# Kernel optimization log

Measured on AMD Instinct MI355X. Metric: run time of the kernel, lower is better.

## Reference

```python
import jax, jax.numpy as jnp
import numpy as np

C_IN = 256
C_INT = C_IN // 2  # inter_channels


def _conv1x1(x, w, b):
    # x: [B, Cin, H, W], w: [Cout, Cin], b: [Cout]
    return jnp.einsum('bchw,oc->bohw', x, w) + b[None, :, None, None]


def setup_inputs() -> dict:
    key = jax.random.key(0)
    ks = jax.random.split(key, 9)
    B, H, W = 8, 64, 64
    s_in = 1.0 / np.sqrt(C_IN)
    s_int = 1.0 / np.sqrt(C_INT)
    return {
        'x': jax.random.normal(ks[0], (B, C_IN, H, W), dtype=jnp.float32),
        'g_w': jax.random.normal(ks[1], (C_INT, C_IN), dtype=jnp.float32) * s_in,
        'g_b': jax.random.normal(ks[2], (C_INT,), dtype=jnp.float32) * s_in,
        'theta_w': jax.random.normal(ks[3], (C_INT, C_IN), dtype=jnp.float32) * s_in,
        'theta_b': jax.random.normal(ks[4], (C_INT,), dtype=jnp.float32) * s_in,
        'phi_w': jax.random.normal(ks[5], (C_INT, C_IN), dtype=jnp.float32) * s_in,
        'phi_b': jax.random.normal(ks[6], (C_INT,), dtype=jnp.float32) * s_in,
        'W_w': jax.random.normal(ks[7], (C_IN, C_INT), dtype=jnp.float32) * s_int,
        'W_b': jax.random.normal(ks[8], (C_IN,), dtype=jnp.float32) * s_int,
    }


def reference(x, g_w, g_b, theta_w, theta_b, phi_w, phi_b, W_w, W_b):
    B, C, H, W = x.shape
    N = H * W
    g_x = _conv1x1(x, g_w, g_b).reshape(B, C_INT, N)        # [B, Ci, N]
    theta_x = _conv1x1(x, theta_w, theta_b).reshape(B, C_INT, N)
    phi_x = _conv1x1(x, phi_w, phi_b).reshape(B, C_INT, N)
    # f[b, i, j] = theta[:, i] . phi[:, j]  (no scaling, per original)
    f = jnp.einsum('bci,bcj->bij', theta_x, phi_x)          # [B, N, N]
    f_div_C = jax.nn.softmax(f, axis=-1)
    y = jnp.einsum('bij,bcj->bci', f_div_C, g_x)            # [B, Ci, N]
    y = y.reshape(B, C_INT, H, W)
    y = _conv1x1(y, W_w, W_b)                               # [B, C, H, W]
    return x + y
```

## Files before the change

### kernel.cpp

```cpp
#include <hip/hip_runtime.h>

typedef _Float16 f16;
typedef _Float16 f16x4 __attribute__((ext_vector_type(4)));
typedef _Float16 f16x8 __attribute__((ext_vector_type(8)));
typedef float f32x4 __attribute__((ext_vector_type(4)));
typedef float f32x16 __attribute__((ext_vector_type(16)));

#define MFMA16(a, b, c) __builtin_amdgcn_mfma_f32_16x16x32_f16(a, b, c, 0, 0, 0)
#define MFMA32(a, b, c) __builtin_amdgcn_mfma_f32_32x32x16_f16(a, b, c, 0, 0, 0)

__device__ __forceinline__ int swzr(int row) { return ((row & 7) << 4) ^ ((row & 8) << 2); }

__global__ __launch_bounds__(256) void wcvt_k(
    const float* __restrict__ tw, const float* __restrict__ pw,
    const float* __restrict__ gw, const float* __restrict__ ww,
    f16* __restrict__ Wall, f16* __restrict__ Wepi) {
  int i = blockIdx.x * 256 + threadIdx.x;
  if (i < 384 * 256) {
    int c = i >> 8, cp = i & 255;
    float v = (c < 128) ? tw[c * 256 + cp]
            : (c < 256) ? pw[(c - 128) * 256 + cp]
                        : gw[(c - 256) * 256 + cp];
    Wall[i] = (f16)v;
  }
  int j = i - 384 * 256;
  if (j >= 0 && j < 256 * 128) Wepi[j] = (f16)ww[j];
}

__global__ __launch_bounds__(256) void proj_k(
    const float* __restrict__ x, const f16* __restrict__ Wall,
    const float* __restrict__ tb, const float* __restrict__ pb,
    const float* __restrict__ gb, f16* __restrict__ Q, f16* __restrict__ K,
    f16* __restrict__ Vt) {
  __shared__ f16 xs[64 * 264];
  __shared__ f16 vs[128 * 65];
  int b = blockIdx.x >> 6, nt = blockIdx.x & 63;
  int nbase = nt * 64;
  int tid = threadIdx.x;

  int nq = tid & 15, kq0 = tid >> 4;
#pragma unroll
  for (int p = 0; p < 4; ++p) {
    int kq = kq0 + 16 * p;
    float4 ld[4];
#pragma unroll
    for (int j = 0; j < 4; ++j)
      ld[j] = *(const float4*)(x + ((size_t)b * 256 + 4 * kq + j) * 4096 + nbase + 4 * nq);
#pragma unroll
    for (int e = 0; e < 4; ++e) {
      f16x4 wv = {(f16)((&ld[0].x)[e]), (f16)((&ld[1].x)[e]), (f16)((&ld[2].x)[e]),
                  (f16)((&ld[3].x)[e])};
      *(f16x4*)(&xs[(4 * nq + e) * 264 + 4 * kq]) = wv;
    }
  }
  __syncthreads();

  int w = tid >> 6, lane = tid & 63;
  int lr = lane & 15, lhi = lane >> 4;
  f16x8 a[8];
#pragma unroll
  for (int ks = 0; ks < 8; ++ks)
    a[ks] = *(const f16x8*)(&xs[(w * 16 + lr) * 264 + ks * 32 + lhi * 8]);
  f32x4 acc[24];
#pragma unroll
  for (int ct = 0; ct < 24; ++ct) {
    acc[ct] = {0.f, 0.f, 0.f, 0.f};
    const f16x8* wr = (const f16x8*)(Wall + (size_t)(ct * 16 + lr) * 256);
#pragma unroll
    for (int ks = 0; ks < 8; ++ks) acc[ct] = MFMA16(a[ks], wr[ks * 4 + lhi], acc[ct]);
  }
  int nloc = w * 16 + lhi * 4;
#pragma unroll
  for (int ct = 0; ct < 24; ++ct) {
    int c = ct * 16 + lr;
    float bias = (c < 128) ? tb[c] : (c < 256) ? pb[c - 128] : gb[c - 256];
#pragma unroll
    for (int r = 0; r < 4; ++r) {
      float v = acc[ct][r] + bias;
      int n = nbase + nloc + r;
      if (c < 128)
        Q[((size_t)b * 4096 + n) * 128 + c] = (f16)v;
      else if (c < 256)
        K[((size_t)b * 4096 + n) * 128 + (c - 128)] = (f16)v;
      else
        vs[(c - 256) * 65 + nloc + r] = (f16)v;
    }
  }
  __syncthreads();
  f16* vo = Vt + (size_t)b * 128 * 4096 + nbase;
  for (int rep = 0; rep < 32; ++rep) {
    int idx = rep * 256 + threadIdx.x;
    int c = idx >> 6, j = idx & 63;
    vo[(size_t)c * 4096 + j] = vs[c * 65 + j];
  }
}

__global__ __launch_bounds__(256, 2) void attn_k(const f16* __restrict__ Q,
                                                 const f16* __restrict__ K,
                                                 const f16* __restrict__ Vt,
                                                 f16* __restrict__ Yp,
                                                 float2* __restrict__ ml) {
  __shared__ f16 Ks[2][64 * 128];
  __shared__ f16 Vs[2][128 * 64];
  const float L = 1.44269504f;
  int swzid = ((blockIdx.x & 7) << 6) | ((int)blockIdx.x >> 3);
  int b = swzid >> 6, rem = swzid & 63;
  int qt = rem >> 1, half = rem & 1;
  int qbase = qt * 128;
  int kvbase = half << 11;
  int tid = threadIdx.x;
  int w = tid >> 6, lane = tid & 63;
  int col = lane & 31, hi = lane >> 5;

  const f16* Qr = Q + ((size_t)b * 4096 + qbase + w * 32 + col) * 128;
  f16x8 bq[8];
#pragma unroll
  for (int ks = 0; ks < 8; ++ks) bq[ks] = *(const f16x8*)(Qr + ks * 16 + hi * 8);

  f32x16 yacc[4];
#pragma unroll
  for (int dt = 0; dt < 4; ++dt)
#pragma unroll
    for (int r = 0; r < 16; ++r) yacc[dt][r] = 0.f;
  float lv[16];
#pragma unroll
  for (int r = 0; r < 16; ++r) lv[r] = 0.f;
  float m = -1e30f, nmL = 1e30f;

  const f16* Kbase = K + (size_t)b * 4096 * 128;
  const f16* Vbase = Vt + (size_t)b * 128 * 4096;

  int krow = tid >> 4, kcolb = (tid & 15) * 16;
  int vrow = tid >> 1, h2 = tid & 1;
  int sv = swzr(vrow);

  {
    const f16* Kt = Kbase + (size_t)kvbase * 128;
    f16x8 kr[4], vr[4];
#pragma unroll
    for (int r = 0; r < 4; ++r) kr[r] = *(const f16x8*)(Kt + (r * 256 + tid) * 8);
#pragma unroll
    for (int u = 0; u < 4; ++u)
      vr[u] = *(const f16x8*)(Vbase + (size_t)vrow * 4096 + kvbase + h2 * 32 + u * 8);
#pragma unroll
    for (int r = 0; r < 4; ++r) {
      int row = r * 16 + krow;
      *(f16x8*)((char*)Ks[0] + row * 256 + (kcolb ^ swzr(row))) = kr[r];
    }
    f16x8 c0, c1, c2, c3;
#pragma unroll
    for (int e = 0; e < 4; ++e) {
      c0[e] = vr[0][e];     c0[4 + e] = vr[1][e];
      c1[e] = vr[0][4 + e]; c1[4 + e] = vr[1][4 + e];
      c2[e] = vr[2][e];     c2[4 + e] = vr[3][e];
      c3[e] = vr[2][4 + e]; c3[4 + e] = vr[3][4 + e];
    }
    char* vb = (char*)Vs[0] + vrow * 128;
    *(f16x8*)(vb + ((h2 * 64 + 0) ^ sv)) = c0;
    *(f16x8*)(vb + ((h2 * 64 + 16) ^ sv)) = c1;
    *(f16x8*)(vb + ((h2 * 64 + 32) ^ sv)) = c2;
    *(f16x8*)(vb + ((h2 * 64 + 48) ^ sv)) = c3;
  }

  for (int t = 0; t < 32; ++t) {
    int cur = t & 1, nxt = cur ^ 1;
    f16x8 kr[4], vr[4];
    bool pf = (t + 1 < 32);
    if (pf) {
      int kv0 = kvbase + (t + 1) * 64;
      const f16* Kt = Kbase + (size_t)kv0 * 128;
#pragma unroll
      for (int r = 0; r < 4; ++r) kr[r] = *(const f16x8*)(Kt + (r * 256 + tid) * 8);
#pragma unroll
      for (int u = 0; u < 4; ++u)
        vr[u] = *(const f16x8*)(Vbase + (size_t)vrow * 4096 + kv0 + h2 * 32 + u * 8);
    }
    __syncthreads();

    f32x16 s2[2];
    __builtin_amdgcn_s_setprio(1);
#pragma unroll
    for (int t2 = 0; t2 < 2; ++t2) {
#pragma unroll
      for (int r = 0; r < 16; ++r) s2[t2][r] = 0.f;
      int row = t2 * 32 + col;
      const char* kb = (const char*)Ks[cur] + row * 256;
      int sk = swzr(row);
#pragma unroll
      for (int ks = 0; ks < 8; ++ks) {
        f16x8 ak = *(const f16x8*)(kb + ((ks * 32 + hi * 16) ^ sk));
        s2[t2] = MFMA32(ak, bq[ks], s2[t2]);
      }
    }
    __builtin_amdgcn_s_setprio(0);

    float v[16];
#pragma unroll
    for (int r = 0; r < 16; ++r) v[r] = fmaxf(s2[0][r], s2[1][r]);
    float t0 = fmaxf(fmaxf(v[0], v[1]), v[2]);
    float t1 = fmaxf(fmaxf(v[3], v[4]), v[5]);
    float t2 = fmaxf(fmaxf(v[6], v[7]), v[8]);
    float t3 = fmaxf(fmaxf(v[9], v[10]), v[11]);
    float t4 = fmaxf(fmaxf(v[12], v[13]), v[14]);
    float u0 = fmaxf(fmaxf(t0, t1), t2);
    float u1 = fmaxf(fmaxf(t3, t4), v[15]);
    float pm = fmaxf(u0, u1);
    pm = fmaxf(pm, __shfl_xor(pm, 32));
    if (pm > m + 8.f) {
      float sc = __expf(m - pm);
      m = pm;
      nmL = -m * L;
#pragma unroll
      for (int r = 0; r < 16; ++r) lv[r] *= sc;
#pragma unroll
      for (int dt = 0; dt < 4; ++dt)
#pragma unroll
        for (int r = 0; r < 16; ++r) yacc[dt][r] *= sc;
    }
#pragma unroll
    for (int t2i = 0; t2i < 2; ++t2i)
#pragma unroll
      for (int r = 0; r < 16; ++r) s2[t2i][r] = exp2f(fmaf(s2[t2i][r], L, nmL));
#pragma unroll
    for (int r = 0; r < 16; ++r) lv[r] += s2[0][r] + s2[1][r];

    f16x8 pfr[4];
#pragma unroll
    for (int t2i = 0; t2i < 2; ++t2i)
#pragma unroll
      for (int k1 = 0; k1 < 2; ++k1) {
        f16x8 f;
#pragma unroll
        for (int c = 0; c < 8; ++c) f[c] = (f16)s2[t2i][8 * k1 + c];
        pfr[t2i * 2 + k1] = f;
      }

    __builtin_amdgcn_s_setprio(1);
#pragma unroll
    for (int kstep = 0; kstep < 4; ++kstep) {
#pragma unroll
      for (int dt = 0; dt < 4; ++dt) {
        int row = dt * 32 + col;
        f16x8 av = *(const f16x8*)((const char*)Vs[cur] + row * 128 +
                                   ((kstep * 32 + hi * 16) ^ swzr(row)));
        yacc[dt] = MFMA32(av, pfr[kstep], yacc[dt]);
      }
    }
    __builtin_amdgcn_s_setprio(0);

    if (pf) {
#pragma unroll
      for (int r = 0; r < 4; ++r) {
        int row = r * 16 + krow;
        *(f16x8*)((char*)Ks[nxt] + row * 256 + (kcolb ^ swzr(row))) = kr[r];
      }
      f16x8 c0, c1, c2, c3;
#pragma unroll
      for (int e = 0; e < 4; ++e) {
        c0[e] = vr[0][e];     c0[4 + e] = vr[1][e];
        c1[e] = vr[0][4 + e]; c1[4 + e] = vr[1][4 + e];
        c2[e] = vr[2][e];     c2[4 + e] = vr[3][e];
        c3[e] = vr[2][4 + e]; c3[4 + e] = vr[3][4 + e];
      }
      char* vb = (char*)Vs[nxt] + vrow * 128;
      *(f16x8*)(vb + ((h2 * 64 + 0) ^ sv)) = c0;
      *(f16x8*)(vb + ((h2 * 64 + 16) ^ sv)) = c1;
      *(f16x8*)(vb + ((h2 * 64 + 32) ^ sv)) = c2;
      *(f16x8*)(vb + ((h2 * 64 + 48) ^ sv)) = c3;
    }
  }

  float l8[8], l4[4];
#pragma unroll
  for (int i = 0; i < 8; ++i) l8[i] = lv[i] + lv[i + 8];
#pragma unroll
  for (int i = 0; i < 4; ++i) l4[i] = l8[i] + l8[i + 4];
  float l = (l4[0] + l4[1]) + (l4[2] + l4[3]);
  l += __shfl_xor(l, 32);

  int rowG = b * 4096 + qbase + w * 32 + col;
  f16* yo = Yp + ((size_t)half * 32768 + rowG) * 128;
  float inv = 1.0f / l;
#pragma unroll
  for (int dt = 0; dt < 4; ++dt)
#pragma unroll
    for (int a = 0; a < 4; ++a) {
      f16x4 ov = {(f16)(yacc[dt][4 * a] * inv), (f16)(yacc[dt][4 * a + 1] * inv),
                  (f16)(yacc[dt][4 * a + 2] * inv), (f16)(yacc[dt][4 * a + 3] * inv)};
      *(f16x4*)(yo + dt * 32 + a * 8 + hi * 4) = ov;
    }
  if (hi == 0) ml[half * 32768 + rowG] = make_float2(m, l);
}

__global__ __launch_bounds__(256) void epi_k(const f16* __restrict__ Yp,
                                             const float2* __restrict__ ml,
                                             const f16* __restrict__ Wepi,
                                             const float* __restrict__ Wb,
                                             const float* __restrict__ x,
                                             float* __restrict__ out) {
  int b = blockIdx.x >> 6, nt = blockIdx.x & 63;
  int nbase = nt * 64;
  int w = threadIdx.x >> 6, lane = threadIdx.x & 63;
  int lr = lane & 15, lhi = lane >> 4;
  const f16* yb1 = Yp + (size_t)32768 * 128;
  f16x8 by[4][4];
#pragma unroll
  for (int n4 = 0; n4 < 4; ++n4) {
    int row = b * 4096 + nbase + n4 * 16 + lr;
    float2 m0 = ml[row], m1 = ml[32768 + row];
    float mm = fmaxf(m0.x, m1.x);
    float w0 = m0.y * __expf(m0.x - mm), w1 = m1.y * __expf(m1.x - mm);
    float inv = 1.f / (w0 + w1);
    w0 *= inv;
    w1 *= inv;
    size_t rb = (size_t)row * 128;
#pragma unroll
    for (int ks = 0; ks < 4; ++ks) {
      int eo = ks * 32 + lhi * 8;
      f16x8 a0 = *(const f16x8*)(Yp + rb + eo);
      f16x8 a1 = *(const f16x8*)(yb1 + rb + eo);
      f16x8 o;
#pragma unroll
      for (int e = 0; e < 8; ++e) o[e] = (f16)(w0 * (float)a0[e] + w1 * (float)a1[e]);
      by[n4][ks] = o;
    }
  }
#pragma unroll
  for (int ot = 0; ot < 4; ++ot) {
    int o0 = w * 64 + ot * 16;
    const f16x8* wr = (const f16x8*)(Wepi + (size_t)(o0 + lr) * 128);
    f16x8 a[4];
#pragma unroll
    for (int ks = 0; ks < 4; ++ks) a[ks] = wr[ks * 4 + lhi];
#pragma unroll
    for (int n4 = 0; n4 < 4; ++n4) {
      f32x4 acc = {0.f, 0.f, 0.f, 0.f};
#pragma unroll
      for (int ks = 0; ks < 4; ++ks) acc = MFMA16(a[ks], by[n4][ks], acc);
#pragma unroll
      for (int r = 0; r < 4; ++r) {
        int o = o0 + lhi * 4 + r;
        int n = nbase + n4 * 16 + lr;
        size_t idx = ((size_t)b * 256 + o) * 4096 + n;
        out[idx] = x[idx] + Wb[o] + acc[r];
      }
    }
  }
}

extern "C" void kernel_launch(void* const* d_in, const int* in_sizes, int n_in,
                              void* d_out, int out_size, void* d_ws, size_t ws_size,
                              hipStream_t stream) {
  const float* x       = (const float*)d_in[0];
  const float* g_w     = (const float*)d_in[1];
  const float* g_b     = (const float*)d_in[2];
  const float* theta_w = (const float*)d_in[3];
  const float* theta_b = (const float*)d_in[4];
  const float* phi_w   = (const float*)d_in[5];
  const float* phi_b   = (const float*)d_in[6];
  const float* W_w     = (const float*)d_in[7];
  const float* W_b     = (const float*)d_in[8];
  float* out = (float*)d_out;

  f16* Q    = (f16*)d_ws;
  f16* Kk   = Q + (size_t)8 * 4096 * 128;
  f16* Vt   = Kk + (size_t)8 * 4096 * 128;
  f16* Wall = Vt + (size_t)8 * 4096 * 128;
  f16* Wepi = Wall + 384 * 256;
  float2* ml = (float2*)(Wepi + 256 * 128);
  f16* Yp   = (f16*)(ml + 2 * 32768);

  wcvt_k<<<512, 256, 0, stream>>>(theta_w, phi_w, g_w, W_w, Wall, Wepi);
  proj_k<<<512, 256, 0, stream>>>(x, Wall, theta_b, phi_b, g_b, Q, Kk, Vt);
  attn_k<<<512, 256, 0, stream>>>(Q, Kk, Vt, Yp, ml);
  epi_k<<<512, 256, 0, stream>>>(Yp, ml, Wepi, W_b, x, out);
}
```

Measured before the change: 186.9 us.

## Split attention KV range four ways, single-buffer LDS, raise occupancy

The attention kernel now splits each query tile's key/value range into four chunks instead of two, launching twice as many blocks, each with half the iterations. Shared memory drops from double to single buffering with two barriers per iteration, and the launch bound rises to three blocks per CU. The row sum now comes from the f16 probabilities via fdot2 rather than sixteen fp32 accumulators. The epilogue merges four partial results, at the cost of extra workspace traffic and exposed load latency without the double buffer.

```diff
diff --git a/kernel.cpp b/kernel.cpp
--- a/kernel.cpp
+++ b/kernel.cpp
@@ -3,11 +3,18 @@
 typedef _Float16 f16;
 typedef _Float16 f16x4 __attribute__((ext_vector_type(4)));
 typedef _Float16 f16x8 __attribute__((ext_vector_type(8)));
+typedef __fp16 h2 __attribute__((ext_vector_type(2)));
 typedef float f32x4 __attribute__((ext_vector_type(4)));
 typedef float f32x16 __attribute__((ext_vector_type(16)));
 
 #define MFMA16(a, b, c) __builtin_amdgcn_mfma_f32_16x16x32_f16(a, b, c, 0, 0, 0)
 #define MFMA32(a, b, c) __builtin_amdgcn_mfma_f32_32x32x16_f16(a, b, c, 0, 0, 0)
+
+#if defined(__has_builtin)
+#if __has_builtin(__builtin_amdgcn_fdot2)
+#define HAS_FDOT2 1
+#endif
+#endif
 
 __device__ __forceinline__ int swzr(int row) { return ((row & 7) << 4) ^ ((row & 8) << 2); }
 
@@ -95,19 +102,19 @@
   }
 }
 
-__global__ __launch_bounds__(256, 2) void attn_k(const f16* __restrict__ Q,
+__global__ __launch_bounds__(256, 3) void attn_k(const f16* __restrict__ Q,
                                                  const f16* __restrict__ K,
                                                  const f16* __restrict__ Vt,
                                                  f16* __restrict__ Yp,
                                                  float2* __restrict__ ml) {
-  __shared__ f16 Ks[2][64 * 128];
-  __shared__ f16 Vs[2][128 * 64];
+  __shared__ f16 Ks[64 * 128];
+  __shared__ f16 Vs[128 * 64];
   const float L = 1.44269504f;
-  int swzid = ((blockIdx.x & 7) << 6) | ((int)blockIdx.x >> 3);
-  int b = swzid >> 6, rem = swzid & 63;
-  int qt = rem >> 1, half = rem & 1;
+  int swzid = ((blockIdx.x & 7) << 7) | ((int)blockIdx.x >> 3);
+  int b = swzid >> 7, rem = swzid & 127;
+  int qt = rem >> 2, s = rem & 3;
   int qbase = qt * 128;
-  int kvbase = half << 11;
+  int kvbase = s << 10;
   int tid = threadIdx.x;
   int w = tid >> 6, lane = tid & 63;
   int col = lane & 31, hi = lane >> 5;
@@ -122,16 +129,14 @@
   for (int dt = 0; dt < 4; ++dt)
 #pragma unroll
     for (int r = 0; r < 16; ++r) yacc[dt][r] = 0.f;
-  float lv[16];
-#pragma unroll
-  for (int r = 0; r < 16; ++r) lv[r] = 0.f;
+  float lv[4] = {0.f, 0.f, 0.f, 0.f};
   float m = -1e30f, nmL = 1e30f;
 
   const f16* Kbase = K + (size_t)b * 4096 * 128;
   const f16* Vbase = Vt + (size_t)b * 128 * 4096;
 
   int krow = tid >> 4, kcolb = (tid & 15) * 16;
-  int vrow = tid >> 1, h2 = tid & 1;
+  int vrow = tid >> 1, h2i = tid & 1;
   int sv = swzr(vrow);
 
   {
@@ -141,11 +146,11 @@
     for (int r = 0; r < 4; ++r) kr[r] = *(const f16x8*)(Kt + (r * 256 + tid) * 8);
 #pragma unroll
     for (int u = 0; u < 4; ++u)
-      vr[u] = *(const f16x8*)(Vbase + (size_t)vrow * 4096 + kvbase + h2 * 32 + u * 8);
+      vr[u] = *(const f16x8*)(Vbase + (size_t)vrow * 4096 + kvbase + h2i * 32 + u * 8);
 #pragma unroll
     for (int r = 0; r < 4; ++r) {
       int row = r * 16 + krow;
-      *(f16x8*)((char*)Ks[0] + row * 256 + (kcolb ^ swzr(row))) = kr[r];
+      *(f16x8*)((char*)Ks + row * 256 + (kcolb ^ swzr(row))) = kr[r];
     }
     f16x8 c0, c1, c2, c3;
 #pragma unroll
@@ -155,17 +160,17 @@
       c2[e] = vr[2][e];     c2[4 + e] = vr[3][e];
       c3[e] = vr[2][4 + e]; c3[4 + e] = vr[3][4 + e];
     }
-    char* vb = (char*)Vs[0] + vrow * 128;
-    *(f16x8*)(vb + ((h2 * 64 + 0) ^ sv)) = c0;
-    *(f16x8*)(vb + ((h2 * 64 + 16) ^ sv)) = c1;
-    *(f16x8*)(vb + ((h2 * 64 + 32) ^ sv)) = c2;
-    *(f16x8*)(vb + ((h2 * 64 + 48) ^ sv)) = c3;
-  }
-
-  for (int t = 0; t < 32; ++t) {
-    int cur = t & 1, nxt = cur ^ 1;
+    char* vb = (char*)Vs + vrow * 128;
+    *(f16x8*)(vb + ((h2i * 64 + 0) ^ sv)) = c0;
+    *(f16x8*)(vb + ((h2i * 64 + 16) ^ sv)) = c1;
+    *(f16x8*)(vb + ((h2i * 64 + 32) ^ sv)) = c2;
+    *(f16x8*)(vb + ((h2i * 64 + 48) ^ sv)) = c3;
+  }
+  __syncthreads();
+
+  for (int t = 0; t < 16; ++t) {
     f16x8 kr[4], vr[4];
-    bool pf = (t + 1 < 32);
+    bool pf = (t + 1 < 16);
     if (pf) {
       int kv0 = kvbase + (t + 1) * 64;
       const f16* Kt = Kbase + (size_t)kv0 * 128;
@@ -173,9 +178,8 @@
       for (int r = 0; r < 4; ++r) kr[r] = *(const f16x8*)(Kt + (r * 256 + tid) * 8);
 #pragma unroll
       for (int u = 0; u < 4; ++u)
-        vr[u] = *(const f16x8*)(Vbase + (size_t)vrow * 4096 + kv0 + h2 * 32 + u * 8);
-    }
-    __syncthreads();
+        vr[u] = *(const f16x8*)(Vbase + (size_t)vrow * 4096 + kv0 + h2i * 32 + u * 8);
+    }
 
     f32x16 s2[2];
     __builtin_amdgcn_s_setprio(1);
@@ -184,7 +188,7 @@
 #pragma unroll
       for (int r = 0; r < 16; ++r) s2[t2][r] = 0.f;
       int row = t2 * 32 + col;
-      const char* kb = (const char*)Ks[cur] + row * 256;
+      const char* kb = (const char*)Ks + row * 256;
       int sk = swzr(row);
 #pragma unroll
       for (int ks = 0; ks < 8; ++ks) {
@@ -194,24 +198,28 @@
     }
     __builtin_amdgcn_s_setprio(0);
 
-    float v[16];
-#pragma unroll
-    for (int r = 0; r < 16; ++r) v[r] = fmaxf(s2[0][r], s2[1][r]);
-    float t0 = fmaxf(fmaxf(v[0], v[1]), v[2]);
-    float t1 = fmaxf(fmaxf(v[3], v[4]), v[5]);
-    float t2 = fmaxf(fmaxf(v[6], v[7]), v[8]);
-    float t3 = fmaxf(fmaxf(v[9], v[10]), v[11]);
-    float t4 = fmaxf(fmaxf(v[12], v[13]), v[14]);
-    float u0 = fmaxf(fmaxf(t0, t1), t2);
-    float u1 = fmaxf(fmaxf(t3, t4), v[15]);
-    float pm = fmaxf(u0, u1);
+    float w0 = fmaxf(fmaxf(s2[0][0], s2[0][1]), s2[0][2]);
+    float w1 = fmaxf(fmaxf(s2[0][3], s2[0][4]), s2[0][5]);
+    float w2 = fmaxf(fmaxf(s2[0][6], s2[0][7]), s2[0][8]);
+    float w3 = fmaxf(fmaxf(s2[0][9], s2[0][10]), s2[0][11]);
+    float w4 = fmaxf(fmaxf(s2[0][12], s2[0][13]), s2[0][14]);
+    float w5 = fmaxf(fmaxf(s2[0][15], s2[1][0]), s2[1][1]);
+    float w6 = fmaxf(fmaxf(s2[1][2], s2[1][3]), s2[1][4]);
+    float w7 = fmaxf(fmaxf(s2[1][5], s2[1][6]), s2[1][7]);
+    float w8 = fmaxf(fmaxf(s2[1][8], s2[1][9]), s2[1][10]);
+    float w9 = fmaxf(fmaxf(s2[1][11], s2[1][12]), s2[1][13]);
+    float wb = fmaxf(s2[1][14], s2[1][15]);
+    float x0 = fmaxf(fmaxf(w0, w1), w2);
+    float x1 = fmaxf(fmaxf(w3, w4), w5);
+    float x2 = fmaxf(fmaxf(w6, w7), w8);
+    float pm = fmaxf(fmaxf(x0, x1), fmaxf(x2, fmaxf(w9, wb)));
     pm = fmaxf(pm, __shfl_xor(pm, 32));
     if (pm > m + 8.f) {
       float sc = __expf(m - pm);
       m = pm;
       nmL = -m * L;
 #pragma unroll
-      for (int r = 0; r < 16; ++r) lv[r] *= sc;
+      for (int i = 0; i < 4; ++i) lv[i] *= sc;
 #pragma unroll
       for (int dt = 0; dt < 4; ++dt)
 #pragma unroll
@@ -221,8 +229,6 @@
     for (int t2i = 0; t2i < 2; ++t2i)
 #pragma unroll
       for (int r = 0; r < 16; ++r) s2[t2i][r] = exp2f(fmaf(s2[t2i][r], L, nmL));
-#pragma unroll
-    for (int r = 0; r < 16; ++r) lv[r] += s2[0][r] + s2[1][r];
 
     f16x8 pfr[4];
 #pragma unroll
@@ -234,6 +240,24 @@
         for (int c = 0; c < 8; ++c) f[c] = (f16)s2[t2i][8 * k1 + c];
         pfr[t2i * 2 + k1] = f;
       }
+#if defined(HAS_FDOT2)
+    {
+      h2 one2 = {1.0f, 1.0f};
+#pragma unroll
+      for (int i = 0; i < 4; ++i) {
+        const h2* pp = (const h2*)&pfr[i];
+#pragma unroll
+        for (int j = 0; j < 4; ++j)
+          lv[j] = __builtin_amdgcn_fdot2(pp[j], one2, lv[j], false);
+      }
+    }
+#else
+#pragma unroll
+    for (int i = 0; i < 4; ++i)
+#pragma unroll
+      for (int j = 0; j < 4; ++j)
+        lv[j] += (float)pfr[i][2 * j] + (float)pfr[i][2 * j + 1];
+#endif
 
     __builtin_amdgcn_s_setprio(1);
 #pragma unroll
@@ -241,18 +265,19 @@
 #pragma unroll
       for (int dt = 0; dt < 4; ++dt) {
         int row = dt * 32 + col;
-        f16x8 av = *(const f16x8*)((const char*)Vs[cur] + row * 128 +
+        f16x8 av = *(const f16x8*)((const char*)Vs + row * 128 +
                                    ((kstep * 32 + hi * 16) ^ swzr(row)));
         yacc[dt] = MFMA32(av, pfr[kstep], yacc[dt]);
       }
     }
     __builtin_amdgcn_s_setprio(0);
 
+    __syncthreads();
     if (pf) {
 #pragma unroll
       for (int r = 0; r < 4; ++r) {
         int row = r * 16 + krow;
-        *(f16x8*)((char*)Ks[nxt] + row * 256 + (kcolb ^ swzr(row))) = kr[r];
+        *(f16x8*)((char*)Ks + row * 256 + (kcolb ^ swzr(row))) = kr[r];
       }
       f16x8 c0, c1, c2, c3;
 #pragma unroll
@@ -262,24 +287,20 @@
         c2[e] = vr[2][e];     c2[4 + e] = vr[3][e];
         c3[e] = vr[2][4 + e]; c3[4 + e] = vr[3][4 + e];
       }
-      char* vb = (char*)Vs[nxt] + vrow * 128;
-      *(f16x8*)(vb + ((h2 * 64 + 0) ^ sv)) = c0;
-      *(f16x8*)(vb + ((h2 * 64 + 16) ^ sv)) = c1;
-      *(f16x8*)(vb + ((h2 * 64 + 32) ^ sv)) = c2;
-      *(f16x8*)(vb + ((h2 * 64 + 48) ^ sv)) = c3;
-    }
-  }
-
-  float l8[8], l4[4];
-#pragma unroll
-  for (int i = 0; i < 8; ++i) l8[i] = lv[i] + lv[i + 8];
-#pragma unroll
-  for (int i = 0; i < 4; ++i) l4[i] = l8[i] + l8[i + 4];
-  float l = (l4[0] + l4[1]) + (l4[2] + l4[3]);
+      char* vb = (char*)Vs + vrow * 128;
+      *(f16x8*)(vb + ((h2i * 64 + 0) ^ sv)) = c0;
+      *(f16x8*)(vb + ((h2i * 64 + 16) ^ sv)) = c1;
+      *(f16x8*)(vb + ((h2i * 64 + 32) ^ sv)) = c2;
+      *(f16x8*)(vb + ((h2i * 64 + 48) ^ sv)) = c3;
+    }
+    __syncthreads();
+  }
+
+  float l = (lv[0] + lv[1]) + (lv[2] + lv[3]);
   l += __shfl_xor(l, 32);
 
   int rowG = b * 4096 + qbase + w * 32 + col;
-  f16* yo = Yp + ((size_t)half * 32768 + rowG) * 128;
+  f16* yo = Yp + ((size_t)s * 32768 + rowG) * 128;
   float inv = 1.0f / l;
 #pragma unroll
   for (int dt = 0; dt < 4; ++dt)
@@ -289,7 +310,7 @@
                   (f16)(yacc[dt][4 * a + 2] * inv), (f16)(yacc[dt][4 * a + 3] * inv)};
       *(f16x4*)(yo + dt * 32 + a * 8 + hi * 4) = ov;
     }
-  if (hi == 0) ml[half * 32768 + rowG] = make_float2(m, l);
+  if (hi == 0) ml[s * 32768 + rowG] = make_float2(m, l);
 }
 
 __global__ __launch_bounds__(256) void epi_k(const f16* __restrict__ Yp,
@@ -302,26 +323,29 @@
   int nbase = nt * 64;
   int w = threadIdx.x >> 6, lane = threadIdx.x & 63;
   int lr = lane & 15, lhi = lane >> 4;
-  const f16* yb1 = Yp + (size_t)32768 * 128;
   f16x8 by[4][4];
 #pragma unroll
   for (int n4 = 0; n4 < 4; ++n4) {
     int row = b * 4096 + nbase + n4 * 16 + lr;
-    float2 m0 = ml[row], m1 = ml[32768 + row];
-    float mm = fmaxf(m0.x, m1.x);
+    float2 m0 = ml[row], m1 = ml[32768 + row], m2 = ml[65536 + row], m3 = ml[98304 + row];
+    float mm = fmaxf(fmaxf(m0.x, m1.x), fmaxf(m2.x, m3.x));
     float w0 = m0.y * __expf(m0.x - mm), w1 = m1.y * __expf(m1.x - mm);
-    float inv = 1.f / (w0 + w1);
-    w0 *= inv;
-    w1 *= inv;
+    float w2 = m2.y * __expf(m2.x - mm), w3 = m3.y * __expf(m3.x - mm);
+    float inv = 1.f / (w0 + w1 + w2 + w3);
+    w0 *= inv; w1 *= inv; w2 *= inv; w3 *= inv;
     size_t rb = (size_t)row * 128;
 #pragma unroll
     for (int ks = 0; ks < 4; ++ks) {
       int eo = ks * 32 + lhi * 8;
       f16x8 a0 = *(const f16x8*)(Yp + rb + eo);
-      f16x8 a1 = *(const f16x8*)(yb1 + rb + eo);
+      f16x8 a1 = *(const f16x8*)(Yp + (size_t)32768 * 128 + rb + eo);
+      f16x8 a2 = *(const f16x8*)(Yp + (size_t)65536 * 128 + rb + eo);
+      f16x8 a3 = *(const f16x8*)(Yp + (size_t)98304 * 128 + rb + eo);
       f16x8 o;
 #pragma unroll
-      for (int e = 0; e < 8; ++e) o[e] = (f16)(w0 * (float)a0[e] + w1 * (float)a1[e]);
+      for (int e = 0; e < 8; ++e)
+        o[e] = (f16)(w0 * (float)a0[e] + w1 * (float)a1[e] + w2 * (float)a2[e] +
+                     w3 * (float)a3[e]);
       by[n4][ks] = o;
     }
   }
@@ -368,10 +392,10 @@
   f16* Wall = Vt + (size_t)8 * 4096 * 128;
   f16* Wepi = Wall + 384 * 256;
   float2* ml = (float2*)(Wepi + 256 * 128);
-  f16* Yp   = (f16*)(ml + 2 * 32768);
+  f16* Yp   = (f16*)(ml + 4 * 32768);
 
   wcvt_k<<<512, 256, 0, stream>>>(theta_w, phi_w, g_w, W_w, Wall, Wepi);
   proj_k<<<512, 256, 0, stream>>>(x, Wall, theta_b, phi_b, g_b, Q, Kk, Vt);
-  attn_k<<<512, 256, 0, stream>>>(Q, Kk, Vt, Yp, ml);
+  attn_k<<<1024, 256, 0, stream>>>(Q, Kk, Vt, Yp, ml);
   epi_k<<<512, 256, 0, stream>>>(Yp, ml, Wepi, W_b, x, out);
 }
```

Measured after the change: 355.5 us. 90.2% more time.
